# Optimization experiments

Hardware: AMD Instinct MI355X
Metric: run time of the kernel (lower is better)

## Reference

```python
import jax, jax.numpy as jnp
import numpy as np

B, L, D, H = 8, 256, 512, 512
NEG_BIG = 1e8  # matches the 100000000.0 mask constant in the original


def setup_inputs() -> dict:
    key = jax.random.key(0)
    k1, k2, k3, k4 = jax.random.split(key, 4)
    enc = jax.random.normal(k1, (B, L, D), dtype=jnp.float32)
    # Glorot-uniform init, matching tf.keras.initializers.GlorotUniform
    s_w = float(np.sqrt(6.0 / (D + H)))
    W_l = jax.random.uniform(k2, (D, H), jnp.float32, -s_w, s_w)
    W_r = jax.random.uniform(k3, (D, H), jnp.float32, -s_w, s_w)
    s_u = float(np.sqrt(6.0 / (H + H)))  # 1-D glorot: fan_in = fan_out = H
    U = jax.random.uniform(k4, (H,), jnp.float32, -s_u, s_u)
    logit_bias = jnp.zeros((1,), jnp.float32)  # bias_initial_value=None -> zeros init
    return {"encoder_output": enc, "W_l": W_l, "W_r": W_r, "U": U, "logit_bias": logit_bias}


def reference(encoder_output, W_l, W_r, U, logit_bias):
    # dot_l[b,i,h], dot_r[b,j,h]
    dot_l = jnp.einsum('bik,kh->bih', encoder_output, W_l)
    dot_r = jnp.einsum('bjk,kh->bjh', encoder_output, W_r)
    # additive biaffine: tanh(dot_l_i + dot_r_j) . U  -> logits[b,i,j]
    final_sum = jnp.tanh(dot_l[:, :, None, :] + dot_r[:, None, :, :])  # [B,L,L,H]
    logits = jnp.einsum('bijh,h->bij', final_sum, U) + logit_bias[0]   # [B,L,L]
    # per-row self-mask (one_hot(i)) applied over all rows at once
    masked = logits - NEG_BIG * jnp.eye(L, dtype=logits.dtype)[None]   # [B,L,L]
    # original returns python lists over i of [B,L]; stack -> [L,B,L]
    mask_scores = jnp.transpose(masked, (1, 0, 2))
    p = jax.nn.sigmoid(mask_scores)
    samples = jax.random.bernoulli(jax.random.key(42), p).astype(jnp.int32)  # [L,B,L]
    # Bernoulli entropy from logits x: p*softplus(-x) + (1-p)*softplus(x)
    entropy = p * jax.nn.softplus(-mask_scores) + (1.0 - p) * jax.nn.softplus(mask_scores)
    return samples, mask_scores, entropy
```

## Files before the change

kernel.cpp:

```cpp
#include <hip/hip_runtime.h>
#include <stdint.h>

#define Bb 8
#define Ll 256
#define Dd 512
#define Hh 512
#define Nout (Ll * Bb * Ll)

#define Kc 2.8853900817779268

#define RNG_PARTITIONABLE 1

typedef __attribute__((ext_vector_type(8))) short bf16x8;
typedef __attribute__((ext_vector_type(4))) float f32x4;

__device__ __forceinline__ uint32_t rotl32(uint32_t v, int s) {
  return (v << s) | (v >> (32 - s));
}
__device__ __forceinline__ void tf_round(uint32_t& x0, uint32_t& x1, int r) {
  x0 += x1;
  x1 = rotl32(x1, r);
  x1 ^= x0;
}
__device__ __forceinline__ uint2 threefry2x32_k042(uint32_t x0, uint32_t x1) {
  const uint32_t k0 = 0u;
  const uint32_t k1 = 42u;
  const uint32_t k2 = 0x1BD11BDAu ^ k0 ^ k1;
  x0 += k0; x1 += k1;
  tf_round(x0, x1, 13); tf_round(x0, x1, 15); tf_round(x0, x1, 26); tf_round(x0, x1, 6);
  x0 += k1; x1 += k2 + 1u;
  tf_round(x0, x1, 17); tf_round(x0, x1, 29); tf_round(x0, x1, 16); tf_round(x0, x1, 24);
  x0 += k2; x1 += k0 + 2u;
  tf_round(x0, x1, 13); tf_round(x0, x1, 15); tf_round(x0, x1, 26); tf_round(x0, x1, 6);
  x0 += k0; x1 += k1 + 3u;
  tf_round(x0, x1, 17); tf_round(x0, x1, 29); tf_round(x0, x1, 16); tf_round(x0, x1, 24);
  x0 += k1; x1 += k2 + 4u;
  tf_round(x0, x1, 13); tf_round(x0, x1, 15); tf_round(x0, x1, 26); tf_round(x0, x1, 6);
  x0 += k2; x1 += k0 + 5u;
  return make_uint2(x0, x1);
}

__device__ __forceinline__ uint32_t rng_bits(uint32_t n) {
#if RNG_PARTITIONABLE
  uint2 o = threefry2x32_k042(0u, n);
  return o.x ^ o.y;
#else
  const uint32_t half = (uint32_t)(Nout / 2);
  if (n < half) {
    uint2 o = threefry2x32_k042(n, n + half);
    return o.x;
  } else {
    uint2 o = threefry2x32_k042(n - half, n);
    return o.y;
  }
#endif
}

__device__ __forceinline__ unsigned short bf16_rne(float f) {
  uint32_t u = __float_as_uint(f);
  u = (u + 0x7fffu + ((u >> 16) & 1u)) >> 16;
  return (unsigned short)u;
}
__device__ __forceinline__ float bf16_tof(unsigned short h) {
  return __uint_as_float(((uint32_t)h) << 16);
}
__device__ __forceinline__ void split3(float a, unsigned short& h,
                                       unsigned short& m, unsigned short& l) {
  h = bf16_rne(a);
  const float r1 = a - bf16_tof(h);
  m = bf16_rne(r1);
  const float r2 = r1 - bf16_tof(m);
  l = bf16_rne(r2);
}

__global__ __launch_bounds__(256) void split_enc(
    const float* __restrict__ enc, unsigned short* __restrict__ ah,
    unsigned short* __restrict__ am, unsigned short* __restrict__ al) {
  const int idx = (blockIdx.x * 256 + threadIdx.x) * 4;
  const float4 v = *(const float4*)(enc + idx);
  ushort4 h4, m4, l4;
  split3(v.x, h4.x, m4.x, l4.x);
  split3(v.y, h4.y, m4.y, l4.y);
  split3(v.z, h4.z, m4.z, l4.z);
  split3(v.w, h4.w, m4.w, l4.w);
  *(ushort4*)(ah + idx) = h4;
  *(ushort4*)(am + idx) = m4;
  *(ushort4*)(al + idx) = l4;
}

__global__ __launch_bounds__(256) void split_wt(
    const float* __restrict__ Wl, const float* __restrict__ Wr,
    unsigned short* __restrict__ wh, unsigned short* __restrict__ wm,
    unsigned short* __restrict__ wl) {
  const int z = blockIdx.z;
  const float* W = z ? Wr : Wl;
  const size_t zo = (size_t)z * Hh * Dd;
  const int k0 = blockIdx.x * 64;
  const int n0 = blockIdx.y * 64;
  __shared__ float tile[64][65];

  const int t = threadIdx.x;
#pragma unroll
  for (int rep = 0; rep < 4; ++rep) {
    const int idx = t + rep * 256;
    const int r = idx >> 4;
    const int c = (idx & 15) * 4;
    const float4 v = *(const float4*)(W + (size_t)(k0 + r) * Hh + n0 + c);
    tile[r][c + 0] = v.x; tile[r][c + 1] = v.y;
    tile[r][c + 2] = v.z; tile[r][c + 3] = v.w;
  }
  __syncthreads();
#pragma unroll
  for (int rep = 0; rep < 4; ++rep) {
    const int idx = t + rep * 256;
    const int rr = idx >> 4;
    const int cc = (idx & 15) * 4;
    ushort4 h4, m4, l4;
    split3(tile[cc + 0][rr], h4.x, m4.x, l4.x);
    split3(tile[cc + 1][rr], h4.y, m4.y, l4.y);
    split3(tile[cc + 2][rr], h4.z, m4.z, l4.z);
    split3(tile[cc + 3][rr], h4.w, m4.w, l4.w);
    const size_t o = zo + (size_t)(n0 + rr) * Dd + k0 + cc;
    *(ushort4*)(wh + o) = h4;
    *(ushort4*)(wm + o) = m4;
    *(ushort4*)(wl + o) = l4;
  }
}

__global__ __launch_bounds__(256) void gemm_mfma(
    const unsigned short* __restrict__ ah, const unsigned short* __restrict__ am,
    const unsigned short* __restrict__ al, const unsigned short* __restrict__ wh,
    const unsigned short* __restrict__ wm, const unsigned short* __restrict__ wl,
    float* __restrict__ el, float* __restrict__ er) {
  const int flat = blockIdx.x;
  const int xcd = flat & 7;
  const int loc = flat >> 3;
  const int z = loc >> 5;
  const int ni = (loc >> 2) & 7;
  const int mi = (xcd << 2) | (loc & 3);
  const size_t zo = (size_t)z * Hh * Dd;
  float* C = z ? er : el;
  const int m0 = mi * 64;
  const int n0 = ni * 64;

  __shared__ unsigned short Asm[2][12 * 512];
  __shared__ unsigned short Bsm[2][12 * 512];

  const int t = threadIdx.x;
  const int lane = t & 63;
  const int wv = t >> 6;
  const int l15 = lane & 15;
  const int kq8 = (lane >> 4) * 8;

  const unsigned short* gp[6];
  size_t go[6];
  int lq[6];
  bool isA[6];
#pragma unroll
  for (int s = 0; s < 6; ++s) {
    const int q = wv * 6 + s;
    if (q < 12) {
      const int p = q >> 2, mt = q & 3;
      gp[s] = (p == 0) ? ah : (p == 1) ? am : al;
      go[s] = (size_t)(m0 + mt * 16 + l15) * Dd + kq8;
      lq[s] = q * 512;
      isA[s] = true;
    } else {
      const int q2 = q - 12;
      const int p = q2 >> 2, nt = q2 & 3;
      gp[s] = (p == 0) ? wh : (p == 1) ? wm : wl;
      go[s] = zo + (size_t)(n0 + nt * 16 + l15) * Dd + kq8;
      lq[s] = q2 * 512;
      isA[s] = false;
    }
  }

  auto stage = [&](int buf, int kc) {
    const int k0 = kc * 32;
#pragma unroll
    for (int s = 0; s < 6; ++s) {
      unsigned short* dst = isA[s] ? &Asm[buf][lq[s]] : &Bsm[buf][lq[s]];
      __builtin_amdgcn_global_load_lds(
          (const __attribute__((address_space(1))) void*)(gp[s] + go[s] + k0),
          (__attribute__((address_space(3))) void*)dst, 16, 0, 0);
    }
  };

  const int mp = wv & 1;
  const int np = wv >> 1;

  f32x4 acc[2][2][2];
#pragma unroll
  for (int mi2 = 0; mi2 < 2; ++mi2)
#pragma unroll
    for (int ni2 = 0; ni2 < 2; ++ni2)
#pragma unroll
      for (int hf = 0; hf < 2; ++hf) acc[mi2][ni2][hf] = (f32x4){0.f, 0.f, 0.f, 0.f};

  stage(0, 0);
  __syncthreads();

  for (int kc = 0; kc < 16; ++kc) {
    const int buf = kc & 1;
    if (kc < 15) stage(buf ^ 1, kc + 1);

    bf16x8 af[2][3], bfr[2][3];
#pragma unroll
    for (int mi2 = 0; mi2 < 2; ++mi2)
#pragma unroll
      for (int p = 0; p < 3; ++p)
        af[mi2][p] = *(const bf16x8*)&Asm[buf][(p * 4 + mp * 2 + mi2) * 512 + lane * 8];
#pragma unroll
    for (int ni2 = 0; ni2 < 2; ++ni2)
#pragma unroll
      for (int p = 0; p < 3; ++p)
        bfr[ni2][p] = *(const bf16x8*)&Bsm[buf][(p * 4 + np * 2 + ni2) * 512 + lane * 8];

    const int hf = kc >> 3;
#pragma unroll
    for (int mi2 = 0; mi2 < 2; ++mi2)
#pragma unroll
      for (int ni2 = 0; ni2 < 2; ++ni2) {
        f32x4 A = acc[mi2][ni2][hf];
        A = __builtin_amdgcn_mfma_f32_16x16x32_bf16(af[mi2][0], bfr[ni2][0], A, 0, 0, 0);
        A = __builtin_amdgcn_mfma_f32_16x16x32_bf16(af[mi2][0], bfr[ni2][1], A, 0, 0, 0);
        A = __builtin_amdgcn_mfma_f32_16x16x32_bf16(af[mi2][1], bfr[ni2][0], A, 0, 0, 0);
        A = __builtin_amdgcn_mfma_f32_16x16x32_bf16(af[mi2][0], bfr[ni2][2], A, 0, 0, 0);
        A = __builtin_amdgcn_mfma_f32_16x16x32_bf16(af[mi2][2], bfr[ni2][0], A, 0, 0, 0);
        A = __builtin_amdgcn_mfma_f32_16x16x32_bf16(af[mi2][1], bfr[ni2][1], A, 0, 0, 0);
        acc[mi2][ni2][hf] = A;
      }
    __syncthreads();
  }

  const int rbase = (lane >> 4) * 4;
#pragma unroll
  for (int mi2 = 0; mi2 < 2; ++mi2) {
    const int mbase = m0 + (mp * 2 + mi2) * 16 + rbase;
#pragma unroll
    for (int ni2 = 0; ni2 < 2; ++ni2) {
      const int n = n0 + (np * 2 + ni2) * 16 + l15;
#pragma unroll
      for (int reg = 0; reg < 4; ++reg) {
        const double s = (double)acc[mi2][ni2][0][reg] + (double)acc[mi2][ni2][1][reg];
        C[(size_t)(mbase + reg) * Hh + n] = __builtin_amdgcn_exp2f((float)(Kc * s));
      }
    }
  }
}

__device__ __forceinline__ void group4_acc(float& S, const float4 a,
                                           const float4 bv, const float4 u) {
  const float d0 = __builtin_fmaf(a.x, bv.x, 1.0f);
  const float d1 = __builtin_fmaf(a.y, bv.y, 1.0f);
  const float d2 = __builtin_fmaf(a.z, bv.z, 1.0f);
  const float d3 = __builtin_fmaf(a.w, bv.w, 1.0f);
  const float p01 = d0 * d1;
  const float p23 = d2 * d3;
  const float D = p01 * p23;
  float n01 = u.x * d1;
  n01 = __builtin_fmaf(u.y, d0, n01);
  float n23 = u.z * d3;
  n23 = __builtin_fmaf(u.w, d2, n23);
  float num = n01 * p23;
  num = __builtin_fmaf(n23, p01, num);
  S = __builtin_fmaf(num, __builtin_amdgcn_rcpf(D), S);
}

__global__ __launch_bounds__(256) void biaffine_part(
    const float* __restrict__ el, const float* __restrict__ er,
    const float* __restrict__ U, float* __restrict__ part) {
  const int flat = blockIdx.x;
  const int b = flat & 7;
  const int loc = flat >> 3;
  const int ks = loc >> 4;
  const int ib = (loc >> 2) & 3;
  const int jb = loc & 3;
  const int i0 = ib * 64;
  const int j0 = jb * 64;
  const int h0 = ks * 64;

  __shared__ float els[64][68];
  __shared__ float ers[64][68];
  __shared__ float us[64];

  const int t = threadIdx.x;
  if (t < 16) *(float4*)&us[t * 4] = *(const float4*)(U + h0 + t * 4);

  const float* elg = el + (size_t)(b * Ll + i0) * Hh + h0;
  const float* erg = er + (size_t)(b * Ll + j0) * Hh + h0;
#pragma unroll
  for (int rep = 0; rep < 4; ++rep) {
    const int idx = t + rep * 256;
    const int r = idx >> 4;
    const int c = (idx & 15) * 4;
    *(float4*)&els[r][c] = *(const float4*)(elg + (size_t)r * Hh + c);
    *(float4*)&ers[r][c] = *(const float4*)(erg + (size_t)r * Hh + c);
  }
  __syncthreads();

  float usl = 0.0f;
#pragma unroll
  for (int q = 0; q < 16; ++q) {
    const float4 u = *(const float4*)&us[q * 4];
    usl += ((u.x + u.y) + u.z) + u.w;
  }

  const int ti = t >> 4;
  const int tj = t & 15;

  float S[4][4];
#pragma unroll
  for (int r = 0; r < 4; ++r)
#pragma unroll
    for (int c = 0; c < 4; ++c) S[r][c] = 0.0f;

  for (int g = 0; g < 16; ++g) {
    const int h = g * 4;
    const float4 u = *(const float4*)&us[h];
    float4 av[4], bv[4];
#pragma unroll
    for (int c = 0; c < 4; ++c) {
      av[c] = *(const float4*)&els[ti + 16 * c][h];
      bv[c] = *(const float4*)&ers[tj + 16 * c][h];
    }
#pragma unroll
    for (int r = 0; r < 4; ++r)
#pragma unroll
      for (int c = 0; c < 4; ++c) group4_acc(S[r][c], av[r], bv[c], u);
  }

  float* pslice = part + (size_t)ks * Nout;
#pragma unroll
  for (int r = 0; r < 4; ++r) {
    const int i = i0 + ti + 16 * r;
#pragma unroll
    for (int c = 0; c < 4; ++c) {
      const int j = j0 + tj + 16 * c;
      const uint32_t n = ((uint32_t)i * Bb + (uint32_t)b) * Ll + (uint32_t)j;
      pslice[n] = __builtin_fmaf(-2.0f, S[r][c], usl);
    }
  }
}

__global__ __launch_bounds__(256) void biaffine_emit(
    const float* __restrict__ part, const float* __restrict__ biasp,
    float* __restrict__ out) {
  const uint32_t n4 = (blockIdx.x * 256u + threadIdx.x) * 4u;
  double s0 = 0.0, s1 = 0.0, s2 = 0.0, s3 = 0.0;
#pragma unroll
  for (int k = 0; k < 8; ++k) {
    const float4 v = *(const float4*)(part + (size_t)k * Nout + n4);
    s0 += (double)v.x;
    s1 += (double)v.y;
    s2 += (double)v.z;
    s3 += (double)v.w;
  }
  const float bias = biasp[0];
  const double sv[4] = {s0, s1, s2, s3};

  float4 samp4, x4, ent4;
  float* sp = &samp4.x;
  float* xp = &x4.x;
  float* ep = &ent4.x;
#pragma unroll
  for (int q = 0; q < 4; ++q) {
    const uint32_t n = n4 + q;
    const int i = (int)(n >> 11);
    const int j = (int)(n & 255u);
    float x = (float)sv[q] + bias;
    if (i == j) x -= 1e8f;

    const double pd = 1.0 / (1.0 + exp(-(double)x));
    const float pf = (float)pd;

    const uint32_t bits = rng_bits(n);
    const float uu = __uint_as_float((bits >> 9) | 0x3f800000u) - 1.0f;
    sp[q] = (uu < pf) ? 1.0f : 0.0f;
    xp[q] = x;

    const float ax = fabsf(x);
    const float l1p = log1pf(expf(-ax));
    const float sp_pos = fmaxf(x, 0.0f) + l1p;
    const float sp_neg = fmaxf(-x, 0.0f) + l1p;
    ep[q] = pf * sp_neg + (1.0f - pf) * sp_pos;
  }
  *(float4*)(out + n4) = samp4;
  *(float4*)(out + Nout + n4) = x4;
  *(float4*)(out + 2 * (size_t)Nout + n4) = ent4;
}

extern "C" void kernel_launch(void* const* d_in, const int* in_sizes, int n_in,
                              void* d_out, int out_size, void* d_ws,
                              size_t ws_size, hipStream_t stream) {
  const float* enc = (const float*)d_in[0];
  const float* Wl = (const float*)d_in[1];
  const float* Wr = (const float*)d_in[2];
  const float* U = (const float*)d_in[3];
  const float* lb = (const float*)d_in[4];
  float* out = (float*)d_out;

  char* w = (char*)d_ws;
  float* el = (float*)w;                      w += (size_t)Bb * Ll * Hh * 4;
  float* er = (float*)w;                      w += (size_t)Bb * Ll * Hh * 4;
  float* part = (float*)w;                    w += (size_t)8 * Nout * 4;
  unsigned short* ah = (unsigned short*)w;    w += (size_t)Bb * Ll * Dd * 2;
  unsigned short* am = (unsigned short*)w;    w += (size_t)Bb * Ll * Dd * 2;
  unsigned short* al = (unsigned short*)w;    w += (size_t)Bb * Ll * Dd * 2;
  unsigned short* wh = (unsigned short*)w;    w += (size_t)2 * Dd * Hh * 2;
  unsigned short* wm = (unsigned short*)w;    w += (size_t)2 * Dd * Hh * 2;
  unsigned short* wl = (unsigned short*)w;    w += (size_t)2 * Dd * Hh * 2;

  split_enc<<<dim3((Bb * Ll * Dd) / 1024), 256, 0, stream>>>(enc, ah, am, al);
  split_wt<<<dim3(Dd / 64, Hh / 64, 2), 256, 0, stream>>>(Wl, Wr, wh, wm, wl);
  gemm_mfma<<<dim3(512, 1, 1), 256, 0, stream>>>(
      ah, am, al, wh, wm, wl, el, er);
  biaffine_part<<<dim3(1024, 1, 1), 256, 0, stream>>>(el, er, U, part);
  biaffine_emit<<<dim3(Nout / 1024), 256, 0, stream>>>(part, lb, out);
}
```

Before: 127.0 us.

## Fuse biaffine partial and emit kernels, merge split kernels into one launch

Merges the two bf16-split kernels into one launch and fuses the H-split biaffine partial kernel with the epilogue kernel. Each block now loops over all eight H chunks with double-buffered LDS staging and accumulates in double registers, then applies sigmoid, RNG sampling and entropy directly. This removes the 8x partial-sum buffer write and read and two kernel launches. In exchange, tiles shrink to 32x32 with 4 outputs per thread, so there is less register reuse per LDS load, the grid drops to 512 blocks, and stores become scalar rather than float4.

```diff
diff --git a/kernel.cpp b/kernel.cpp
--- a/kernel.cpp
+++ b/kernel.cpp
@@ -73,33 +73,40 @@
   l = bf16_rne(r2);
 }
 
-__global__ __launch_bounds__(256) void split_enc(
-    const float* __restrict__ enc, unsigned short* __restrict__ ah,
-    unsigned short* __restrict__ am, unsigned short* __restrict__ al) {
-  const int idx = (blockIdx.x * 256 + threadIdx.x) * 4;
-  const float4 v = *(const float4*)(enc + idx);
-  ushort4 h4, m4, l4;
-  split3(v.x, h4.x, m4.x, l4.x);
-  split3(v.y, h4.y, m4.y, l4.y);
-  split3(v.z, h4.z, m4.z, l4.z);
-  split3(v.w, h4.w, m4.w, l4.w);
-  *(ushort4*)(ah + idx) = h4;
-  *(ushort4*)(am + idx) = m4;
-  *(ushort4*)(al + idx) = l4;
-}
-
-__global__ __launch_bounds__(256) void split_wt(
-    const float* __restrict__ Wl, const float* __restrict__ Wr,
+__global__ __launch_bounds__(256) void split_all(
+    const float* __restrict__ enc, const float* __restrict__ Wl,
+    const float* __restrict__ Wr, unsigned short* __restrict__ ah,
+    unsigned short* __restrict__ am, unsigned short* __restrict__ al,
     unsigned short* __restrict__ wh, unsigned short* __restrict__ wm,
     unsigned short* __restrict__ wl) {
-  const int z = blockIdx.z;
+  __shared__ float tile[64][65];
+  const int bx = blockIdx.x;
+  const int t = threadIdx.x;
+
+  if (bx < 1024) {
+    const int idx = (bx * 256 + t) * 4;
+    const float4 v = *(const float4*)(enc + idx);
+    ushort4 h4, m4, l4;
+    split3(v.x, h4.x, m4.x, l4.x);
+    split3(v.y, h4.y, m4.y, l4.y);
+    split3(v.z, h4.z, m4.z, l4.z);
+    split3(v.w, h4.w, m4.w, l4.w);
+    *(ushort4*)(ah + idx) = h4;
+    *(ushort4*)(am + idx) = m4;
+    *(ushort4*)(al + idx) = l4;
+    return;
+  }
+
+  const int id = bx - 1024;
+  const int z = id >> 6;
+  const int rest = id & 63;
+  const int kb = rest >> 3;
+  const int nb = rest & 7;
   const float* W = z ? Wr : Wl;
   const size_t zo = (size_t)z * Hh * Dd;
-  const int k0 = blockIdx.x * 64;
-  const int n0 = blockIdx.y * 64;
-  __shared__ float tile[64][65];
-
-  const int t = threadIdx.x;
+  const int k0 = kb * 64;
+  const int n0 = nb * 64;
+
 #pragma unroll
   for (int rep = 0; rep < 4; ++rep) {
     const int idx = t + rep * 256;
@@ -267,127 +274,133 @@
   S = __builtin_fmaf(num, __builtin_amdgcn_rcpf(D), S);
 }
 
-__global__ __launch_bounds__(256) void biaffine_part(
+__global__ __launch_bounds__(256) void biaffine_fused(
     const float* __restrict__ el, const float* __restrict__ er,
-    const float* __restrict__ U, float* __restrict__ part) {
+    const float* __restrict__ U, const float* __restrict__ biasp,
+    float* __restrict__ out) {
   const int flat = blockIdx.x;
   const int b = flat & 7;
   const int loc = flat >> 3;
-  const int ks = loc >> 4;
-  const int ib = (loc >> 2) & 3;
-  const int jb = loc & 3;
-  const int i0 = ib * 64;
-  const int j0 = jb * 64;
-  const int h0 = ks * 64;
-
-  __shared__ float els[64][68];
-  __shared__ float ers[64][68];
-  __shared__ float us[64];
+  const int ib = loc >> 3;
+  const int jb = loc & 7;
+  const int i0 = ib * 32;
+  const int j0 = jb * 32;
+
+  __shared__ float els[2][32][68];
+  __shared__ float ers[2][32][68];
+  __shared__ float us[512];
 
   const int t = threadIdx.x;
-  if (t < 16) *(float4*)&us[t * 4] = *(const float4*)(U + h0 + t * 4);
-
-  const float* elg = el + (size_t)(b * Ll + i0) * Hh + h0;
-  const float* erg = er + (size_t)(b * Ll + j0) * Hh + h0;
-#pragma unroll
-  for (int rep = 0; rep < 4; ++rep) {
-    const int idx = t + rep * 256;
-    const int r = idx >> 4;
-    const int c = (idx & 15) * 4;
-    *(float4*)&els[r][c] = *(const float4*)(elg + (size_t)r * Hh + c);
-    *(float4*)&ers[r][c] = *(const float4*)(erg + (size_t)r * Hh + c);
-  }
+  if (t < 128) *(float4*)&us[t * 4] = *(const float4*)(U + t * 4);
+
+  const float* elg = el + (size_t)(b * Ll + i0) * Hh;
+  const float* erg = er + (size_t)(b * Ll + j0) * Hh;
+
+  float4 ea[2], eb[2];
+  const int sr[2] = {t >> 4, (t + 256) >> 4};
+  const int sc = (t & 15) * 4;
+
+  auto load_regs = [&](int ks) {
+    const int h0 = ks * 64;
+#pragma unroll
+    for (int rep = 0; rep < 2; ++rep) {
+      ea[rep] = *(const float4*)(elg + (size_t)sr[rep] * Hh + h0 + sc);
+      eb[rep] = *(const float4*)(erg + (size_t)sr[rep] * Hh + h0 + sc);
+    }
+  };
+  auto write_lds = [&](int buf) {
+#pragma unroll
+    for (int rep = 0; rep < 2; ++rep) {
+      *(float4*)&els[buf][sr[rep]][sc] = ea[rep];
+      *(float4*)&ers[buf][sr[rep]][sc] = eb[rep];
+    }
+  };
+
+  load_regs(0);
+  write_lds(0);
   __syncthreads();
-
-  float usl = 0.0f;
-#pragma unroll
-  for (int q = 0; q < 16; ++q) {
-    const float4 u = *(const float4*)&us[q * 4];
-    usl += ((u.x + u.y) + u.z) + u.w;
-  }
 
   const int ti = t >> 4;
   const int tj = t & 15;
 
-  float S[4][4];
-#pragma unroll
-  for (int r = 0; r < 4; ++r)
-#pragma unroll
-    for (int c = 0; c < 4; ++c) S[r][c] = 0.0f;
-
-  for (int g = 0; g < 16; ++g) {
-    const int h = g * 4;
-    const float4 u = *(const float4*)&us[h];
-    float4 av[4], bv[4];
-#pragma unroll
-    for (int c = 0; c < 4; ++c) {
-      av[c] = *(const float4*)&els[ti + 16 * c][h];
-      bv[c] = *(const float4*)&ers[tj + 16 * c][h];
-    }
-#pragma unroll
-    for (int r = 0; r < 4; ++r)
-#pragma unroll
-      for (int c = 0; c < 4; ++c) group4_acc(S[r][c], av[r], bv[c], u);
-  }
-
-  float* pslice = part + (size_t)ks * Nout;
-#pragma unroll
-  for (int r = 0; r < 4; ++r) {
+  double xd[2][2];
+#pragma unroll
+  for (int r = 0; r < 2; ++r)
+#pragma unroll
+    for (int c = 0; c < 2; ++c) xd[r][c] = 0.0;
+
+  for (int ks = 0; ks < 8; ++ks) {
+    const int buf = ks & 1;
+    if (ks < 7) load_regs(ks + 1);
+
+    const int h0 = ks * 64;
+    float usl = 0.0f;
+#pragma unroll
+    for (int q = 0; q < 16; ++q) {
+      const float4 u = *(const float4*)&us[h0 + q * 4];
+      usl += ((u.x + u.y) + u.z) + u.w;
+    }
+
+    float S[2][2];
+#pragma unroll
+    for (int r = 0; r < 2; ++r)
+#pragma unroll
+      for (int c = 0; c < 2; ++c) S[r][c] = 0.0f;
+
+#pragma unroll
+    for (int g = 0; g < 16; ++g) {
+      const int h = g * 4;
+      const float4 u = *(const float4*)&us[h0 + h];
+      float4 av[2], bv[2];
+#pragma unroll
+      for (int r = 0; r < 2; ++r) av[r] = *(const float4*)&els[buf][ti + 16 * r][h];
+#pragma unroll
+      for (int c = 0; c < 2; ++c) bv[c] = *(const float4*)&ers[buf][tj + 16 * c][h];
+#pragma unroll
+      for (int r = 0; r < 2; ++r)
+#pragma unroll
+        for (int c = 0; c < 2; ++c) group4_acc(S[r][c], av[r], bv[c], u);
+    }
+
+#pragma unroll
+    for (int r = 0; r < 2; ++r)
+#pragma unroll
+      for (int c = 0; c < 2; ++c)
+        xd[r][c] += (double)__builtin_fmaf(-2.0f, S[r][c], usl);
+
+    if (ks < 7) {
+      write_lds(buf ^ 1);
+      __syncthreads();
+    }
+  }
+
+  const float bias = biasp[0];
+#pragma unroll
+  for (int r = 0; r < 2; ++r) {
     const int i = i0 + ti + 16 * r;
 #pragma unroll
-    for (int c = 0; c < 4; ++c) {
+    for (int c = 0; c < 2; ++c) {
       const int j = j0 + tj + 16 * c;
       const uint32_t n = ((uint32_t)i * Bb + (uint32_t)b) * Ll + (uint32_t)j;
-      pslice[n] = __builtin_fmaf(-2.0f, S[r][c], usl);
-    }
-  }
-}
-
-__global__ __launch_bounds__(256) void biaffine_emit(
-    const float* __restrict__ part, const float* __restrict__ biasp,
-    float* __restrict__ out) {
-  const uint32_t n4 = (blockIdx.x * 256u + threadIdx.x) * 4u;
-  double s0 = 0.0, s1 = 0.0, s2 = 0.0, s3 = 0.0;
-#pragma unroll
-  for (int k = 0; k < 8; ++k) {
-    const float4 v = *(const float4*)(part + (size_t)k * Nout + n4);
-    s0 += (double)v.x;
-    s1 += (double)v.y;
-    s2 += (double)v.z;
-    s3 += (double)v.w;
-  }
-  const float bias = biasp[0];
-  const double sv[4] = {s0, s1, s2, s3};
-
-  float4 samp4, x4, ent4;
-  float* sp = &samp4.x;
-  float* xp = &x4.x;
-  float* ep = &ent4.x;
-#pragma unroll
-  for (int q = 0; q < 4; ++q) {
-    const uint32_t n = n4 + q;
-    const int i = (int)(n >> 11);
-    const int j = (int)(n & 255u);
-    float x = (float)sv[q] + bias;
-    if (i == j) x -= 1e8f;
-
-    const double pd = 1.0 / (1.0 + exp(-(double)x));
-    const float pf = (float)pd;
-
-    const uint32_t bits = rng_bits(n);
-    const float uu = __uint_as_float((bits >> 9) | 0x3f800000u) - 1.0f;
-    sp[q] = (uu < pf) ? 1.0f : 0.0f;
-    xp[q] = x;
-
-    const float ax = fabsf(x);
-    const float l1p = log1pf(expf(-ax));
-    const float sp_pos = fmaxf(x, 0.0f) + l1p;
-    const float sp_neg = fmaxf(-x, 0.0f) + l1p;
-    ep[q] = pf * sp_neg + (1.0f - pf) * sp_pos;
-  }
-  *(float4*)(out + n4) = samp4;
-  *(float4*)(out + Nout + n4) = x4;
-  *(float4*)(out + 2 * (size_t)Nout + n4) = ent4;
+      float x = (float)xd[r][c] + bias;
+      if (i == j) x -= 1e8f;
+
+      const double pd = 1.0 / (1.0 + exp(-(double)x));
+      const float pf = (float)pd;
+
+      const uint32_t bits = rng_bits(n);
+      const float uu = __uint_as_float((bits >> 9) | 0x3f800000u) - 1.0f;
+
+      const float ax = fabsf(x);
+      const float l1p = log1pf(expf(-ax));
+      const float sp_pos = fmaxf(x, 0.0f) + l1p;
+      const float sp_neg = fmaxf(-x, 0.0f) + l1p;
+
+      out[n] = (uu < pf) ? 1.0f : 0.0f;
+      out[Nout + n] = x;
+      out[2 * (size_t)Nout + n] = pf * sp_neg + (1.0f - pf) * sp_pos;
+    }
+  }
 }
 
 extern "C" void kernel_launch(void* const* d_in, const int* in_sizes, int n_in,
@@ -403,7 +416,6 @@
   char* w = (char*)d_ws;
   float* el = (float*)w;                      w += (size_t)Bb * Ll * Hh * 4;
   float* er = (float*)w;                      w += (size_t)Bb * Ll * Hh * 4;
-  float* part = (float*)w;                    w += (size_t)8 * Nout * 4;
   unsigned short* ah = (unsigned short*)w;    w += (size_t)Bb * Ll * Dd * 2;
   unsigned short* am = (unsigned short*)w;    w += (size_t)Bb * Ll * Dd * 2;
   unsigned short* al = (unsigned short*)w;    w += (size_t)Bb * Ll * Dd * 2;
@@ -411,10 +423,9 @@
   unsigned short* wm = (unsigned short*)w;    w += (size_t)2 * Dd * Hh * 2;
   unsigned short* wl = (unsigned short*)w;    w += (size_t)2 * Dd * Hh * 2;
 
-  split_enc<<<dim3((Bb * Ll * Dd) / 1024), 256, 0, stream>>>(enc, ah, am, al);
-  split_wt<<<dim3(Dd / 64, Hh / 64, 2), 256, 0, stream>>>(Wl, Wr, wh, wm, wl);
+  split_all<<<dim3(1024 + 128), 256, 0, stream>>>(enc, Wl, Wr, ah, am, al,
+                                                  wh, wm, wl);
   gemm_mfma<<<dim3(512, 1, 1), 256, 0, stream>>>(
       ah, am, al, wh, wm, wl, el, er);
-  biaffine_part<<<dim3(1024, 1, 1), 256, 0, stream>>>(el, er, U, part);
-  biaffine_emit<<<dim3(Nout / 1024), 256, 0, stream>>>(part, lb, out);
-}
+  biaffine_fused<<<dim3(512, 1, 1), 256, 0, stream>>>(el, er, U, lb, out);
+}
```

After: 155.0 us. 1.22x slower.
